# Kernel optimization log

Hardware: AMD Instinct MI355X
Metric: run time of the kernel (lower is better)

## Reference

```python
import jax, jax.numpy as jnp
import numpy as np

T, B, D = 512, 16, 512
H, DH, DI, L = 8, 64, 2048, 4
EPS = 1e-6
SCALE = 1.0 / DH ** 0.5
NEG_INF = -1e9


def _ln(x, g, b):
    m = jnp.mean(x, axis=-1, keepdims=True)
    v = jnp.var(x, axis=-1, keepdims=True)
    return (x - m) * jax.lax.rsqrt(v + EPS) * g + b


def _pos_emb(pos_seq):
    inv_freq = 1.0 / (10000.0 ** (jnp.arange(0, D, 2, dtype=jnp.float32) / D))
    s = pos_seq[:, None] * inv_freq[None, :]  # (rlen, D/2)
    return jnp.concatenate([jnp.sin(s), jnp.cos(s)], axis=-1)  # (rlen, D)


def _rel_shift(x, klen):
    # faithful reshape-slice trick: (q, r, b, n) -> view as (r, q, b, n), drop first, back to (q, r-1, b, n)
    q, r, b, n = x.shape
    x = x.reshape(r, q, b, n)[1:].reshape(q, r - 1, b, n)
    return x[:, :klen]


def _layer(h, r, r_w_bias, r_r_bias, attn_mask, qkv_w, r_net_w, o_w,
           ln1_g, ln1_b, w1, b1, w2, b2, ln2_g, ln2_b):
    qlen, bsz, _ = h.shape
    rlen = r.shape[0]
    w_heads = jnp.einsum('ibd,de->ibe', h, qkv_w)
    q, k, v = jnp.split(w_heads, 3, axis=-1)
    q = q.reshape(qlen, bsz, H, DH)
    k = k.reshape(qlen, bsz, H, DH)
    v = v.reshape(qlen, bsz, H, DH)
    rk = jnp.einsum('jbd,de->jbe', r, r_net_w).reshape(rlen, bsz, H, DH)
    AC = jnp.einsum('ibnd,jbnd->ijbn', q + r_w_bias, k)
    BD = _rel_shift(jnp.einsum('ibnd,jbnd->ijbn', q + r_r_bias, rk), qlen)
    score = (AC + BD) * SCALE
    score = jnp.where(attn_mask[None, :, :, None], NEG_INF, score)
    prob = jax.nn.softmax(score, axis=1)
    vec = jnp.einsum('ijbn,jbnd->ibnd', prob, v).reshape(qlen, bsz, H * DH)
    out = _ln(h + jnp.einsum('ibe,ed->ibd', vec, o_w), ln1_g, ln1_b)
    ff = jnp.maximum(jnp.einsum('ibd,df->ibf', out, w1) + b1, 0.0)
    ff = jnp.einsum('ibf,fd->ibd', ff, w2) + b2
    return _ln(out + ff, ln2_g, ln2_b)


def setup_inputs() -> dict:
    key = jax.random.key(0)
    ks = jax.random.split(key, 12)
    s = 0.02
    lengths = jax.random.randint(ks[0], (B,), T // 2, T + 1)
    seq_mask = jnp.arange(T)[None, :] < lengths[:, None]  # (B, T) bool, True = real token
    return {
        'h': jax.random.normal(ks[1], (B, T, D), jnp.float32),
        'seq_mask': seq_mask,
        'r_w_bias': jax.random.normal(ks[2], (H, DH), jnp.float32) * s,
        'r_r_bias': jax.random.normal(ks[3], (H, DH), jnp.float32) * s,
        'top_ln_g': jnp.ones((D,), jnp.float32),
        'top_ln_b': jnp.zeros((D,), jnp.float32),
        'qkv_w': jax.random.normal(ks[4], (L, D, 3 * H * DH), jnp.float32) * s,
        'r_net_w': jax.random.normal(ks[5], (L, D, H * DH), jnp.float32) * s,
        'o_w': jax.random.normal(ks[6], (L, H * DH, D), jnp.float32) * s,
        'attn_ln_g': jnp.ones((L, D), jnp.float32),
        'attn_ln_b': jnp.zeros((L, D), jnp.float32),
        'ff_w1': jax.random.normal(ks[7], (L, D, DI), jnp.float32) * s,
        'ff_b1': jnp.zeros((L, DI), jnp.float32),
        'ff_w2': jax.random.normal(ks[8], (L, DI, D), jnp.float32) * s,
        'ff_b2': jnp.zeros((L, D), jnp.float32),
        'ff_ln_g': jnp.ones((L, D), jnp.float32),
        'ff_ln_b': jnp.zeros((L, D), jnp.float32),
    }


def reference(h, seq_mask, r_w_bias, r_r_bias, top_ln_g, top_ln_b, qkv_w, r_net_w, o_w,
              attn_ln_g, attn_ln_b, ff_w1, ff_b1, ff_w2, ff_b2, ff_ln_g, ff_ln_b):
    h = jnp.transpose(h, (1, 0, 2))            # (T, B, D)
    attn_mask = ~jnp.transpose(seq_mask, (1, 0))  # (T, B), True = padding
    fw = _pos_emb(jnp.arange(T, -T, -1, dtype=h.dtype))
    bw = _pos_emb(jnp.arange(-T, T, 1, dtype=h.dtype))
    pos = jnp.concatenate([
        jnp.broadcast_to(fw[:, None, :], (2 * T, B // 2, D)),
        jnp.broadcast_to(bw[:, None, :], (2 * T, B - B // 2, D)),
    ], axis=1)                                 # (2T, B, D)
    h = _ln(h, top_ln_g, top_ln_b)
    hids = [h]
    out = h
    for i in range(L):
        out = _layer(out, pos, r_w_bias, r_r_bias, attn_mask,
                     qkv_w[i], r_net_w[i], o_w[i], attn_ln_g[i], attn_ln_b[i],
                     ff_w1[i], ff_b1[i], ff_w2[i], ff_b2[i], ff_ln_g[i], ff_ln_b[i])
        hids.append(out)
    out = jnp.transpose(out, (1, 0, 2))
    hids = tuple(jnp.transpose(x, (1, 0, 2)) for x in hids)
    return (out, hids)
```

## Files before the change

kernel.cpp:

```cpp
#include <hip/hip_runtime.h>
#include <cstddef>


typedef unsigned short u16;
typedef short s16x8 __attribute__((ext_vector_type(8)));
typedef unsigned short u16x8 __attribute__((ext_vector_type(8)));
typedef float f32x4 __attribute__((ext_vector_type(4)));

__device__ __forceinline__ u16 f2bf(float f) {
  unsigned int u = __float_as_uint(f);
  u += 0x7fffu + ((u >> 16) & 1u);
  return (u16)(u >> 16);
}
__device__ __forceinline__ float bf2f(u16 u) {
  return __uint_as_float((unsigned int)u << 16);
}

__device__ __forceinline__ f32x4 mfma16(s16x8 a, s16x8 b, f32x4 c) {
  return __builtin_amdgcn_mfma_f32_16x16x32_bf16(a, b, c, 0, 0, 0);
}

__device__ __forceinline__ void gl2lds16(const u16* g, u16* l) {
  __builtin_amdgcn_global_load_lds(
      (const __attribute__((address_space(1))) unsigned int*)g,
      (__attribute__((address_space(3))) unsigned int*)l, 16, 0, 0);
}

template <int MODE, int TN>
__launch_bounds__(256) __global__
void gemm_bt(const u16* __restrict__ A, const u16* __restrict__ Bt,
             int M, int N, int K,
             void* p0, void* p1, void* p2, void* p3,
             const float* __restrict__ p4, const float* __restrict__ p5) {
  (void)M;
  constexpr int NT = TN / 32;
  __shared__ u16 As[4096];
  __shared__ u16 Bs[TN * 32];
  const int tid = threadIdx.x;
  const int lane = tid & 63;
  const int w = tid >> 6;
  const int quad = lane >> 4, l15 = lane & 15;
  const int m0 = blockIdx.y << 7, n0 = blockIdx.x * TN;

  if constexpr (MODE == 0) {
    A += (size_t)blockIdx.z * 524288;
    p0 = (void*)((u16*)p0 + (size_t)blockIdx.z * 524288);
  }

  f32x4 acc[4][NT];
#pragma unroll
  for (int a = 0; a < 4; ++a)
#pragma unroll
    for (int b = 0; b < NT; ++b) {
      f32x4 z = {0.f, 0.f, 0.f, 0.f};
      acc[a][b] = z;
    }

  const int slot0 = w * 64 + lane;
  const int rA = slot0 >> 2, cA = (slot0 & 3) * 8;
  const u16* gA0 = A + (size_t)(m0 + rA) * K + cA;
  const u16* gA1 = A + (size_t)(m0 + 64 + rA) * K + cA;
  const u16* gB0 = Bt + (size_t)(n0 + rA) * K + cA;
  const u16* gB1 = Bt + (size_t)(n0 + 64 + rA) * K + cA;
  u16* lA0 = &As[w * 512];
  u16* lA1 = &As[(4 + w) * 512];
  u16* lB0 = &Bs[w * 512];
  u16* lB1 = &Bs[(4 + w) * 512];

  const int wm = (w >> 1) << 6, wn = (w & 1) * (NT * 16);
  const int nk = K >> 5;
  for (int kt = 0; kt < nk; ++kt) {
    const int k0 = kt << 5;
    gl2lds16(gA0 + k0, lA0);
    gl2lds16(gA1 + k0, lA1);
    gl2lds16(gB0 + k0, lB0);
    if constexpr (TN == 128) gl2lds16(gB1 + k0, lB1);
    __syncthreads();
    s16x8 af[4], bfg[NT];
#pragma unroll
    for (int t = 0; t < 4; ++t)
      af[t] = *(const s16x8*)&As[(wm + t * 16 + l15) * 32 + quad * 8];
#pragma unroll
    for (int t = 0; t < NT; ++t)
      bfg[t] = *(const s16x8*)&Bs[(wn + t * 16 + l15) * 32 + quad * 8];
#pragma unroll
    for (int mt = 0; mt < 4; ++mt)
#pragma unroll
      for (int nt = 0; nt < NT; ++nt)
        acc[mt][nt] = mfma16(af[mt], bfg[nt], acc[mt][nt]);
    __syncthreads();
  }

#pragma unroll
  for (int mt = 0; mt < 4; ++mt) {
#pragma unroll
    for (int nt = 0; nt < NT; ++nt) {
#pragma unroll
      for (int r = 0; r < 4; ++r) {
        const int row = m0 + wm + mt * 16 + quad * 4 + r;
        const int col = n0 + wn + nt * 16 + l15;
        const float v = acc[mt][nt][r];
        if constexpr (MODE == 0) {
          const int hn = col >> 6, d = col & 63;
          ((u16*)p0)[((size_t)hn * 1024 + row) * 64 + d] = f2bf(v);
        } else if constexpr (MODE == 1) {
          const int i = row >> 4, b = row & 15;
          const int which = col >> 9, hn = (col >> 6) & 7, d = col & 63;
          const int bn = b * 8 + hn;
          const size_t idx = ((size_t)bn * 512 + i) * 64 + d;
          if (which == 0) {
            ((u16*)p0)[idx] = f2bf(v + p4[hn * 64 + d]);
            ((u16*)p1)[idx] = f2bf(v + p5[hn * 64 + d]);
          } else if (which == 1) {
            ((u16*)p2)[idx] = f2bf(v);
          } else {
            ((u16*)p3)[idx] = f2bf(v);
          }
        } else if constexpr (MODE == 2) {
          ((float*)p0)[(size_t)row * N + col] =
              v + ((const float*)p1)[(size_t)row * N + col];
        } else if constexpr (MODE == 3) {
          ((float*)p0)[(size_t)row * N + col] =
              v + ((const float*)p1)[(size_t)row * N + col] +
              ((const float*)p2)[col];
        } else {
          float t = v + ((const float*)p1)[col];
          ((u16*)p0)[(size_t)row * N + col] = f2bf(t > 0.f ? t : 0.f);
        }
      }
    }
  }
}

__launch_bounds__(256) __global__
void transpose_w_kernel(const float* __restrict__ qkv, const float* __restrict__ rnet,
                        const float* __restrict__ ow, const float* __restrict__ w1,
                        const float* __restrict__ w2, u16* __restrict__ dst) {
  const int type = blockIdx.z, l = blockIdx.y, tile = blockIdx.x;
  int R, C;
  const float* src;
  u16* out;
  switch (type) {
    case 0: R = 512; C = 1536; src = qkv + (size_t)l * 786432; out = dst + (size_t)l * 786432; break;
    case 1: R = 512; C = 512;  src = rnet + (size_t)l * 262144; out = dst + 3145728 + (size_t)l * 262144; break;
    case 2: R = 512; C = 512;  src = ow + (size_t)l * 262144;   out = dst + 4194304 + (size_t)l * 262144; break;
    case 3: R = 512; C = 2048; src = w1 + (size_t)l * 1048576;  out = dst + 5242880 + (size_t)l * 1048576; break;
    default: R = 2048; C = 512; src = w2 + (size_t)l * 1048576; out = dst + 9437184 + (size_t)l * 1048576; break;
  }
  const int tC = C >> 6;
  const int tR = R >> 6;
  if (tile >= tC * tR) return;
  const int r0 = (tile / tC) << 6, c0 = (tile % tC) << 6;
  __shared__ float tb[64][65];
  const int tid = threadIdx.x;
  const int rr = tid >> 2, cc = (tid & 3) << 4;
#pragma unroll
  for (int j = 0; j < 4; ++j) {
    f32x4 u = *(const f32x4*)(src + (size_t)(r0 + rr) * C + c0 + cc + j * 4);
    tb[rr][cc + j * 4 + 0] = u[0];
    tb[rr][cc + j * 4 + 1] = u[1];
    tb[rr][cc + j * 4 + 2] = u[2];
    tb[rr][cc + j * 4 + 3] = u[3];
  }
  __syncthreads();
  u16x8 o0, o1;
#pragma unroll
  for (int j = 0; j < 8; ++j) o0[j] = f2bf(tb[cc + j][rr]);
#pragma unroll
  for (int j = 0; j < 8; ++j) o1[j] = f2bf(tb[cc + 8 + j][rr]);
  *(u16x8*)(out + (size_t)(c0 + rr) * R + r0 + cc) = o0;
  *(u16x8*)(out + (size_t)(c0 + rr) * R + r0 + cc + 8) = o1;
}

__launch_bounds__(256) __global__
void posemb_kernel(u16* __restrict__ r_bf) {
  const int idx = blockIdx.x * 256 + threadIdx.x;
  const int d = idx & 511, j = (idx >> 9) & 1023, g = idx >> 19;
  const float pos = g ? (float)(j - 512) : (float)(512 - j);
  const int dp = d & 255;
  const float invf = expf((float)dp * (-9.210340371976184f / 256.f));
  const float v = pos * invf;
  r_bf[idx] = f2bf((d < 256) ? sinf(v) : cosf(v));
}

__launch_bounds__(256) __global__
void transpose_v_kernel(const u16* __restrict__ Vb, u16* __restrict__ Vt) {
  const int bn = blockIdx.y, j0 = blockIdx.x << 6;
  __shared__ u16 tb[64][72];
  const int tid = threadIdx.x;
#pragma unroll
  for (int q = 0; q < 2; ++q) {
    const int s = q * 256 + tid;
    const int jj = s >> 3, c = s & 7;
    u16x8 u = *(const u16x8*)(Vb + ((size_t)bn * 512 + j0 + jj) * 64 + c * 8);
    *(u16x8*)&tb[jj][c * 8] = u;
  }
  __syncthreads();
#pragma unroll
  for (int q = 0; q < 2; ++q) {
    const int s = q * 256 + tid;
    const int d = s >> 3, c = s & 7;
    u16x8 o;
#pragma unroll
    for (int e = 0; e < 8; ++e) o[e] = tb[c * 8 + e][d];
    *(u16x8*)(Vt + ((size_t)bn * 64 + d) * 512 + j0 + c * 8) = o;
  }
}

__launch_bounds__(256) __global__
void attn_kernel(const u16* __restrict__ Qw, const u16* __restrict__ Qr,
                 const u16* __restrict__ Kb, const u16* __restrict__ Vt,
                 const u16* __restrict__ rkb, const int* __restrict__ smask,
                 u16* __restrict__ vecb) {
  __shared__ float maskf[512];
  __shared__ u16 Ks[4096];
  __shared__ u16 Vts[4096];
  __shared__ u16 Band[8192];
  __shared__ u16 UN[5376];

  const int tid = threadIdx.x, lane = tid & 63, w = tid >> 6;
  const int quad = lane >> 4, l15 = lane & 15;
  const int bn = blockIdx.y, b = bn >> 3, n = bn & 7;
  const int g = (b >= 8) ? 1 : 0;
  const int i0 = blockIdx.x << 6;

  for (int j = tid; j < 512; j += 256)
    maskf[j] = smask[b * 512 + j] ? 0.f : -1e9f;

  const u16* qwp = Qw + ((size_t)bn * 512 + i0 + w * 16 + l15) * 64 + quad * 8;
  const u16* qrp = Qr + ((size_t)bn * 512 + i0 + w * 16 + l15) * 64 + quad * 8;
  const s16x8 qw0 = *(const s16x8*)qwp, qw1 = *(const s16x8*)(qwp + 32);
  const s16x8 qr0 = *(const s16x8*)qrp, qr1 = *(const s16x8*)(qrp + 32);

  const u16* kbase = Kb + (size_t)bn * (512 * 64);
  const u16* vbase = Vt + (size_t)bn * (64 * 512);
  const u16* rkg = rkb + (size_t)(g * 8 + n) * (1024 * 64);

  const int s0 = w * 64 + lane;
  const int rl = s0 >> 3;
  const int cd = ((s0 & 7) ^ (rl & 7)) * 8;
  u16* lK0 = &Ks[w * 512];
  u16* lK1 = &Ks[(4 + w) * 512];
  u16* lV0 = &Vts[w * 512];
  u16* lV1 = &Vts[(4 + w) * 512];
  u16* lBq[4] = {&Band[w * 512], &Band[(4 + w) * 512], &Band[(8 + w) * 512],
                 &Band[(12 + w) * 512]};
  u16* bwv = &UN[w * 1344];
  u16* pwv = bwv;

  const int sw8 = ((quad ^ (l15 & 7)) * 8);
  const int sw8b = (((quad ^ (l15 & 7)) ^ 4) * 8);

  f32x4 O[4];
  float m_st[4], l_st[4];
#pragma unroll
  for (int t = 0; t < 4; ++t) {
    f32x4 z = {0.f, 0.f, 0.f, 0.f};
    O[t] = z;
    m_st[t] = -1e30f;
    l_st[t] = 0.f;
  }

  for (int jt = 0; jt < 8; ++jt) {
    const int j0 = jt << 6;
    const int jr0 = 449 + j0 - i0;
    __syncthreads();
    gl2lds16(kbase + (size_t)(j0 + rl) * 64 + cd, lK0);
    gl2lds16(kbase + (size_t)(j0 + 32 + rl) * 64 + cd, lK1);
    gl2lds16(vbase + (size_t)rl * 512 + j0 + cd, lV0);
    gl2lds16(vbase + (size_t)(rl + 32) * 512 + j0 + cd, lV1);
#pragma unroll
    for (int q = 0; q < 4; ++q) {
      int rrow = jr0 + q * 32 + rl;
      rrow = rrow < 1023 ? rrow : 1023;
      gl2lds16(rkg + (size_t)rrow * 64 + cd, lBq[q]);
    }
    __syncthreads();

    f32x4 ac[4];
#pragma unroll
    for (int t = 0; t < 4; ++t) {
      f32x4 z = {0.f, 0.f, 0.f, 0.f};
      ac[t] = z;
      s16x8 k0f = *(const s16x8*)&Ks[(t * 16 + l15) * 64 + sw8];
      s16x8 k1f = *(const s16x8*)&Ks[(t * 16 + l15) * 64 + sw8b];
      ac[t] = mfma16(qw0, k0f, ac[t]);
      ac[t] = mfma16(qw1, k1f, ac[t]);
    }
    const int bb0 = 48 - w * 16;
#pragma unroll
    for (int t = 0; t < 5; ++t) {
      f32x4 z = {0.f, 0.f, 0.f, 0.f};
      f32x4 bd = z;
      s16x8 b0f = *(const s16x8*)&Band[(bb0 + t * 16 + l15) * 64 + sw8];
      s16x8 b1f = *(const s16x8*)&Band[(bb0 + t * 16 + l15) * 64 + sw8b];
      bd = mfma16(qr0, b0f, bd);
      bd = mfma16(qr1, b1f, bd);
#pragma unroll
      for (int r = 0; r < 4; ++r)
        bwv[(quad * 4 + r) * 84 + t * 16 + l15] = f2bf(bd[r]);
    }

    float pv[4][4];
#pragma unroll
    for (int t = 0; t < 4; ++t) {
#pragma unroll
      for (int r = 0; r < 4; ++r) {
        const int mi = quad * 4 + r;
        const int nj = t * 16 + l15;
        pv[t][r] = (ac[t][r] + bf2f(bwv[mi * 84 + 15 + nj - mi])) * 0.125f +
                   maskf[j0 + nj];
      }
    }
#pragma unroll
    for (int r = 0; r < 4; ++r) {
      float mx = fmaxf(fmaxf(pv[0][r], pv[1][r]), fmaxf(pv[2][r], pv[3][r]));
#pragma unroll
      for (int xm = 1; xm < 16; xm <<= 1) mx = fmaxf(mx, __shfl_xor(mx, xm));
      const float mn = fmaxf(m_st[r], mx);
      const float al = __expf(m_st[r] - mn);
      m_st[r] = mn;
      float rs = 0.f;
#pragma unroll
      for (int t = 0; t < 4; ++t) {
        pv[t][r] = __expf(pv[t][r] - mn);
        rs += pv[t][r];
      }
#pragma unroll
      for (int xm = 1; xm < 16; xm <<= 1) rs += __shfl_xor(rs, xm);
      l_st[r] = l_st[r] * al + rs;
#pragma unroll
      for (int t = 0; t < 4; ++t) O[t][r] *= al;
    }
#pragma unroll
    for (int t = 0; t < 4; ++t)
#pragma unroll
      for (int r = 0; r < 4; ++r)
        pwv[(quad * 4 + r) * 68 + t * 16 + l15] = f2bf(pv[t][r]);
#pragma unroll
    for (int ks = 0; ks < 2; ++ks) {
      s16x8 pf = *(const s16x8*)&pwv[l15 * 68 + ks * 32 + quad * 8];
#pragma unroll
      for (int td = 0; td < 4; ++td) {
        s16x8 vf = *(const s16x8*)&Vts[(td * 16 + l15) * 64 +
                                       (ks == 0 ? sw8 : sw8b)];
        O[td] = mfma16(pf, vf, O[td]);
      }
    }
  }

#pragma unroll
  for (int td = 0; td < 4; ++td) {
#pragma unroll
    for (int r = 0; r < 4; ++r) {
      const int i = i0 + w * 16 + quad * 4 + r;
      const float val = O[td][r] / l_st[r];
      vecb[((size_t)i * 16 + b) * 512 + n * 64 + td * 16 + l15] = f2bf(val);
    }
  }
}

__launch_bounds__(256) __global__
void ln_kernel(const float* __restrict__ src, int src_is_bt,
               const float* __restrict__ gw, const float* __restrict__ bww,
               float* __restrict__ dst32, u16* __restrict__ dstbf,
               float* __restrict__ o1, float* __restrict__ o2) {
  const int row = blockIdx.x * 4 + (threadIdx.x >> 6);
  const int lane = threadIdx.x & 63;
  const int i = row >> 4, b = row & 15;
  const float* x = src + (src_is_bt ? ((size_t)b * 512 + i) * 512 : (size_t)row * 512);
  f32x4 u0 = *(const f32x4*)(x + lane * 8);
  f32x4 u1 = *(const f32x4*)(x + lane * 8 + 4);
  float s = u0[0] + u0[1] + u0[2] + u0[3] + u1[0] + u1[1] + u1[2] + u1[3];
  float sq = u0[0] * u0[0] + u0[1] * u0[1] + u0[2] * u0[2] + u0[3] * u0[3] +
             u1[0] * u1[0] + u1[1] * u1[1] + u1[2] * u1[2] + u1[3] * u1[3];
  for (int m = 1; m < 64; m <<= 1) {
    s += __shfl_xor(s, m);
    sq += __shfl_xor(sq, m);
  }
  const float mean = s * (1.f / 512.f);
  const float var = sq * (1.f / 512.f) - mean * mean;
  const float rs = rsqrtf(var + 1e-6f);
  f32x4 g0 = *(const f32x4*)(gw + lane * 8);
  f32x4 g1 = *(const f32x4*)(gw + lane * 8 + 4);
  f32x4 b0 = *(const f32x4*)(bww + lane * 8);
  f32x4 b1 = *(const f32x4*)(bww + lane * 8 + 4);
  f32x4 y0, y1;
#pragma unroll
  for (int k = 0; k < 4; ++k) {
    y0[k] = (u0[k] - mean) * rs * g0[k] + b0[k];
    y1[k] = (u1[k] - mean) * rs * g1[k] + b1[k];
  }
  const size_t o_ib = (size_t)row * 512 + lane * 8;
  const size_t o_tb = ((size_t)b * 512 + i) * 512 + lane * 8;
  if (dst32) {
    *(f32x4*)(dst32 + o_ib) = y0;
    *(f32x4*)(dst32 + o_ib + 4) = y1;
  }
  if (dstbf) {
    u16x8 ov;
#pragma unroll
    for (int k = 0; k < 4; ++k) {
      ov[k] = f2bf(y0[k]);
      ov[k + 4] = f2bf(y1[k]);
    }
    *(u16x8*)(dstbf + o_ib) = ov;
  }
  if (o1) {
    *(f32x4*)(o1 + o_tb) = y0;
    *(f32x4*)(o1 + o_tb + 4) = y1;
  }
  if (o2) {
    *(f32x4*)(o2 + o_tb) = y0;
    *(f32x4*)(o2 + o_tb + 4) = y1;
  }
}

extern "C" void kernel_launch(void* const* d_in, const int* in_sizes, int n_in,
                              void* d_out, int out_size, void* d_ws, size_t ws_size,
                              hipStream_t stream) {
  (void)in_sizes; (void)n_in; (void)out_size; (void)ws_size;
  const float* h_in = (const float*)d_in[0];
  const int* smask = (const int*)d_in[1];
  const float* rwb = (const float*)d_in[2];
  const float* rrb = (const float*)d_in[3];
  const float* top_g = (const float*)d_in[4];
  const float* top_b = (const float*)d_in[5];
  const float* qkv_w = (const float*)d_in[6];
  const float* rnet_w = (const float*)d_in[7];
  const float* o_w = (const float*)d_in[8];
  const float* attn_g = (const float*)d_in[9];
  const float* attn_b = (const float*)d_in[10];
  const float* w1 = (const float*)d_in[11];
  const float* b1 = (const float*)d_in[12];
  const float* w2 = (const float*)d_in[13];
  const float* b2 = (const float*)d_in[14];
  const float* ff_g = (const float*)d_in[15];
  const float* ff_b = (const float*)d_in[16];
  float* out = (float*)d_out;
  const size_t BTD = 4194304;

  char* ws = (char*)d_ws;
  size_t off = 0;
  auto alloc = [&](size_t bytes) {
    void* p = ws + off;
    off += (bytes + 255) & ~(size_t)255;
    return p;
  };
  u16* wT = (u16*)alloc(13631488ull * 2);
  u16* r_bf = (u16*)alloc(2ull * 1024 * 512 * 2);
  u16* rkb = (u16*)alloc(2ull * 8 * 1024 * 64 * 2);
  u16* Qw = (u16*)alloc(8ull << 20);
  u16* Qr = (u16*)alloc(8ull << 20);
  u16* Kb = (u16*)alloc(8ull << 20);
  u16* Vt = (u16*)alloc(8ull << 20);
  u16* vecb = (u16*)alloc(8ull << 20);
  u16* Xbf = (u16*)alloc(8ull << 20);
  u16* ffbf = (u16*)alloc(32ull << 20);
  float* hcur = (float*)alloc(16ull << 20);
  float* tmp = (float*)Qw;
  float* mid = (float*)Kb;
  u16* Vb = ffbf;

  dim3 blk(256);
  transpose_w_kernel<<<dim3(256, 4, 5), blk, 0, stream>>>(qkv_w, rnet_w, o_w, w1, w2, wT);
  posemb_kernel<<<dim3(4096), blk, 0, stream>>>(r_bf);
  ln_kernel<<<dim3(2048), blk, 0, stream>>>(h_in, 1, top_g, top_b, hcur, Xbf,
                                            out + BTD, (float*)nullptr);

  for (int l = 0; l < 4; ++l) {
    u16* qkvT = wT + (size_t)l * 786432;
    u16* rnetT = wT + 3145728 + (size_t)l * 262144;
    u16* oT = wT + 4194304 + (size_t)l * 262144;
    u16* w1T = wT + 5242880 + (size_t)l * 1048576;
    u16* w2T = wT + 9437184 + (size_t)l * 1048576;

    gemm_bt<0, 64><<<dim3(8, 8, 2), blk, 0, stream>>>(
        r_bf, rnetT, 1024, 512, 512,
        rkb, nullptr, nullptr, nullptr, nullptr, nullptr);

    gemm_bt<1, 128><<<dim3(12, 64), blk, 0, stream>>>(
        Xbf, qkvT, 8192, 1536, 512, Qw, Qr, Kb, Vb, rwb, rrb);

    transpose_v_kernel<<<dim3(8, 128), blk, 0, stream>>>(Vb, Vt);

    attn_kernel<<<dim3(8, 128), blk, 0, stream>>>(Qw, Qr, Kb, Vt, rkb, smask, vecb);

    gemm_bt<2, 64><<<dim3(8, 64), blk, 0, stream>>>(
        vecb, oT, 8192, 512, 512, tmp, hcur, nullptr, nullptr, nullptr, nullptr);

    ln_kernel<<<dim3(2048), blk, 0, stream>>>(tmp, 0, attn_g + l * 512, attn_b + l * 512,
                                              mid, Xbf, (float*)nullptr, (float*)nullptr);

    gemm_bt<4, 128><<<dim3(16, 64), blk, 0, stream>>>(
        Xbf, w1T, 8192, 2048, 512, ffbf, (void*)(b1 + (size_t)l * 2048),
        nullptr, nullptr, nullptr, nullptr);

    gemm_bt<3, 64><<<dim3(8, 64), blk, 0, stream>>>(
        ffbf, w2T, 8192, 512, 2048, tmp, mid, (void*)(b2 + (size_t)l * 512),
        nullptr, nullptr, nullptr);

    ln_kernel<<<dim3(2048), blk, 0, stream>>>(
        tmp, 0, ff_g + l * 512, ff_b + l * 512, hcur, Xbf,
        out + (size_t)(2 + l) * BTD, (l == 3) ? out : (float*)nullptr);
  }
}
```

Before: 1.154 ms.

## Skip fully padded key tiles and do the rel-shift with lane shuffles

The attention kernel now holds the sequence mask as per-lane bitmasks in registers instead of an LDS float array. It skips 64-key tiles whose keys are all padding. The relative-position shift of the BD scores now uses cross-lane shuffles from register fragments rather than a round trip through LDS, which also keeps BD in fp32 instead of rounding to bf16. The P tile gets an XOR-swizzled LDS layout in place of padded rows, to cut bank conflicts and LDS use. Skipping tiles is exact because masked keys get zero weight, but rows whose keys are all padding would behave differently.

After: 1.080 ms. -6.4%, faster.

```diff
diff --git a/kernel.cpp b/kernel.cpp
--- a/kernel.cpp
+++ b/kernel.cpp
@@ -212,11 +212,10 @@
                  const u16* __restrict__ Kb, const u16* __restrict__ Vt,
                  const u16* __restrict__ rkb, const int* __restrict__ smask,
                  u16* __restrict__ vecb) {
-  __shared__ float maskf[512];
   __shared__ u16 Ks[4096];
   __shared__ u16 Vts[4096];
   __shared__ u16 Band[8192];
-  __shared__ u16 UN[5376];
+  __shared__ u16 Ps[4096];
 
   const int tid = threadIdx.x, lane = tid & 63, w = tid >> 6;
   const int quad = lane >> 4, l15 = lane & 15;
@@ -224,8 +223,15 @@
   const int g = (b >= 8) ? 1 : 0;
   const int i0 = blockIdx.x << 6;
 
-  for (int j = tid; j < 512; j += 256)
-    maskf[j] = smask[b * 512 + j] ? 0.f : -1e9f;
+  unsigned mbits = 0;
+  const int* smb = smask + b * 512 + l15;
+#pragma unroll
+  for (int s = 0; s < 32; ++s)
+    if (smb[s * 16]) mbits |= 1u << s;
+  unsigned vmask = 0;
+#pragma unroll
+  for (int jt = 0; jt < 8; ++jt)
+    if (__any((int)((mbits >> (jt * 4)) & 15u))) vmask |= 1u << jt;
 
   const u16* qwp = Qw + ((size_t)bn * 512 + i0 + w * 16 + l15) * 64 + quad * 8;
   const u16* qrp = Qr + ((size_t)bn * 512 + i0 + w * 16 + l15) * 64 + quad * 8;
@@ -245,11 +251,18 @@
   u16* lV1 = &Vts[(4 + w) * 512];
   u16* lBq[4] = {&Band[w * 512], &Band[(4 + w) * 512], &Band[(8 + w) * 512],
                  &Band[(12 + w) * 512]};
-  u16* bwv = &UN[w * 1344];
-  u16* pwv = bwv;
+  u16* pwv = &Ps[w * 1024];
 
   const int sw8 = ((quad ^ (l15 & 7)) * 8);
   const int sw8b = (((quad ^ (l15 & 7)) ^ 4) * 8);
+
+  int sl[4], hisel[4];
+#pragma unroll
+  for (int r = 0; r < 4; ++r) {
+    const int e = 15 + l15 - quad * 4 - r;
+    sl[r] = (quad << 4) | (e & 15);
+    hisel[r] = e >> 4;
+  }
 
   f32x4 O[4];
   float m_st[4], l_st[4];
@@ -262,6 +275,7 @@
   }
 
   for (int jt = 0; jt < 8; ++jt) {
+    if (!((vmask >> jt) & 1u)) continue;
     const int j0 = jt << 6;
     const int jr0 = 449 + j0 - i0;
     __syncthreads();
@@ -288,28 +302,28 @@
       ac[t] = mfma16(qw1, k1f, ac[t]);
     }
     const int bb0 = 48 - w * 16;
+    f32x4 bd[5];
 #pragma unroll
     for (int t = 0; t < 5; ++t) {
       f32x4 z = {0.f, 0.f, 0.f, 0.f};
-      f32x4 bd = z;
       s16x8 b0f = *(const s16x8*)&Band[(bb0 + t * 16 + l15) * 64 + sw8];
       s16x8 b1f = *(const s16x8*)&Band[(bb0 + t * 16 + l15) * 64 + sw8b];
-      bd = mfma16(qr0, b0f, bd);
-      bd = mfma16(qr1, b1f, bd);
-#pragma unroll
-      for (int r = 0; r < 4; ++r)
-        bwv[(quad * 4 + r) * 84 + t * 16 + l15] = f2bf(bd[r]);
-    }
+      bd[t] = mfma16(qr1, b1f, mfma16(qr0, b0f, z));
+    }
+    float sh[5][4];
+#pragma unroll
+    for (int t = 0; t < 5; ++t)
+#pragma unroll
+      for (int r = 0; r < 4; ++r) sh[t][r] = __shfl(bd[t][r], sl[r]);
 
     float pv[4][4];
 #pragma unroll
     for (int t = 0; t < 4; ++t) {
+      const float mk = ((mbits >> (jt * 4 + t)) & 1u) ? 0.f : -1e9f;
 #pragma unroll
       for (int r = 0; r < 4; ++r) {
-        const int mi = quad * 4 + r;
-        const int nj = t * 16 + l15;
-        pv[t][r] = (ac[t][r] + bf2f(bwv[mi * 84 + 15 + nj - mi])) * 0.125f +
-                   maskf[j0 + nj];
+        const float bdv = hisel[r] ? sh[t + 1][r] : sh[t][r];
+        pv[t][r] = (ac[t][r] + bdv) * 0.125f + mk;
       }
     }
 #pragma unroll
@@ -335,11 +349,15 @@
 #pragma unroll
     for (int t = 0; t < 4; ++t)
 #pragma unroll
-      for (int r = 0; r < 4; ++r)
-        pwv[(quad * 4 + r) * 68 + t * 16 + l15] = f2bf(pv[t][r]);
+      for (int r = 0; r < 4; ++r) {
+        const int row = quad * 4 + r, col = t * 16 + l15;
+        pwv[row * 64 + ((((col >> 3) ^ row) & 7) << 3) + (col & 7)] =
+            f2bf(pv[t][r]);
+      }
 #pragma unroll
     for (int ks = 0; ks < 2; ++ks) {
-      s16x8 pf = *(const s16x8*)&pwv[l15 * 68 + ks * 32 + quad * 8];
+      const int ch = (((ks * 4 + quad) ^ l15) & 7) << 3;
+      s16x8 pf = *(const s16x8*)&pwv[l15 * 64 + ch];
 #pragma unroll
       for (int td = 0; td < 4; ++td) {
         s16x8 vf = *(const s16x8*)&Vts[(td * 16 + l15) * 64 +
```
